# Kernel tuning notes

Measured on AMD Instinct MI355X. Metric: run time of the kernel, lower is better.

The kernel has to match this reference:

```python
import jax, jax.numpy as jnp
import numpy as np

B, S, Hd = 4, 2048, 1024
NH, D = 16, 64

def setup_inputs() -> dict:
    key = jax.random.key(0)
    ks = jax.random.split(key, 8)
    scale = 0.02
    return {
        "hidden_states": jax.random.normal(ks[0], (B, S, Hd), dtype=jnp.float32),
        "attention_mask": jnp.zeros((B, 1, 1, S), dtype=jnp.float32),
        "relations": jax.random.normal(ks[1], (1, 1, S, D), dtype=jnp.float32),
        "Wq": jax.random.normal(ks[2], (Hd, Hd), dtype=jnp.float32) * scale,
        "bq": jnp.zeros((Hd,), dtype=jnp.float32),
        "Wk": jax.random.normal(ks[3], (Hd, Hd), dtype=jnp.float32) * scale,
        "bk": jnp.zeros((Hd,), dtype=jnp.float32),
        "Wv": jax.random.normal(ks[4], (Hd, Hd), dtype=jnp.float32) * scale,
        "bv": jnp.zeros((Hd,), dtype=jnp.float32),
    }

def _heads(x):  # [B,S,Hd] -> [B,NH,S,D]
    return x.reshape(x.shape[0], x.shape[1], NH, D).transpose(0, 2, 1, 3)

def _rotate_half_interleaved(x):
    # stack([-x_odd, x_even], -1).reshape_as(x)
    return jnp.stack([-x[..., 1::2], x[..., ::2]], axis=-1).reshape(x.shape)

def reference(hidden_states, attention_mask, relations, Wq, bq, Wk, bk, Wv, bv):
    q = _heads(hidden_states @ Wq.T + bq)
    k = _heads(hidden_states @ Wk.T + bk)
    v = _heads(hidden_states @ Wv.T + bv)

    # interleaved rotary: cos from odd slots, sin from even slots, each repeated x2
    cos_pos = jnp.repeat(relations[..., 1::2], 2, axis=-1)  # [1,1,S,D]
    sin_pos = jnp.repeat(relations[..., ::2], 2, axis=-1)
    q = q * cos_pos + _rotate_half_interleaved(q) * sin_pos
    k = k * cos_pos + _rotate_half_interleaved(k) * sin_pos

    scores = jnp.einsum("bhqd,bhkd->bhqk", q, k) / jnp.sqrt(jnp.float32(D))
    scores = scores + attention_mask
    probs = jax.nn.softmax(scores, axis=-1)
    ctx = jnp.einsum("bhqk,bhkd->bhqd", probs, v)
    return ctx.transpose(0, 2, 1, 3).reshape(hidden_states.shape[0], hidden_states.shape[1], NH * D)
```

## Files before the change

kernel.cpp:

```cpp
#include <hip/hip_runtime.h>

typedef __attribute__((ext_vector_type(8))) short short8;
typedef __attribute__((ext_vector_type(4))) float f32x4;
typedef __attribute__((ext_vector_type(4))) unsigned int u32x4;
typedef __attribute__((ext_vector_type(2))) unsigned int u32x2;
typedef __attribute__((ext_vector_type(4))) unsigned short u16x4;

#define NHEADS 16
#define DHEAD 64
#define SEQ 2048
#define BATCH 4
#define HD 1024
#define MTOT 8192

static __device__ __forceinline__ unsigned short f2b(float x) {
  unsigned u = __builtin_bit_cast(unsigned, x);
  u += 0x7fffu + ((u >> 16) & 1u);
  return (unsigned short)(u >> 16);
}

static __device__ __forceinline__ unsigned pk2h(float lo, float hi) {
  unsigned a = __builtin_bit_cast(unsigned, lo) + 0x8000u;
  unsigned b = __builtin_bit_cast(unsigned, hi) + 0x8000u;
  return (a >> 16) | (b & 0xffff0000u);
}

static __device__ __forceinline__ void gll16(const void* g, void* l) {
  __builtin_amdgcn_global_load_lds(
      (const __attribute__((address_space(1))) unsigned int*)g,
      (__attribute__((address_space(3))) unsigned int*)l, 16, 0, 0);
}

__global__ void cvt_bf16(const float* __restrict__ src,
                         unsigned short* __restrict__ dst, int n4) {
  int i = blockIdx.x * blockDim.x + threadIdx.x;
  if (i < n4) {
    f32x4 v = ((const f32x4*)src)[i];
    u16x4 o;
    o[0] = f2b(v[0]); o[1] = f2b(v[1]); o[2] = f2b(v[2]); o[3] = f2b(v[3]);
    ((u16x4*)dst)[i] = o;
  }
}

#define WQ4 (HD * HD / 4)
__global__ void prep(const float* __restrict__ Wq, const float* __restrict__ Wk,
                     const float* __restrict__ Wv, const float* __restrict__ mask,
                     unsigned short* __restrict__ Wb,
                     unsigned short* __restrict__ Wm) {
  int i = blockIdx.x * blockDim.x + threadIdx.x;
  if (i < 3 * WQ4) {
    int rg = i / WQ4;
    int idx = i - rg * WQ4;
    const float* src = (rg == 0) ? Wq : (rg == 1) ? Wk : Wv;
    f32x4 v = ((const f32x4*)src)[idx];
    u16x4 o;
    o[0] = f2b(v[0]); o[1] = f2b(v[1]); o[2] = f2b(v[2]); o[3] = f2b(v[3]);
    ((u16x4*)(Wb + (size_t)rg * HD * HD))[idx] = o;
  } else {
    int j = i - 3 * WQ4;
    f32x4 v = ((const f32x4*)mask)[j];
    u16x4 o;
    o[0] = f2b(__expf(v[0])); o[1] = f2b(__expf(v[1]));
    o[2] = f2b(__expf(v[2])); o[3] = f2b(__expf(v[3]));
    ((u16x4*)Wm)[j] = o;
  }
}

__global__ __launch_bounds__(256) void qkv_gemm(
    const unsigned short* __restrict__ X,
    const unsigned short* __restrict__ Wall,
    const float* __restrict__ bq, const float* __restrict__ bk,
    const float* __restrict__ bv,
    const float* __restrict__ rel,
    const float* __restrict__ mask,
    unsigned short* __restrict__ Qo,
    unsigned short* __restrict__ Ko,
    unsigned short* __restrict__ Vt) {
  __shared__ __align__(16) unsigned short As[2][128 * 64];
  __shared__ __align__(16) unsigned short Bs[2][128 * 64];

  const int t = threadIdx.x;
  const int lane = t & 63;
  const int w = t >> 6;

  const int n = blockIdx.x;
  const int xcd = n & 7;
  const int li = n >> 3;
  const int bx = xcd * 8 + (li & 7);
  const int pp = li >> 3;
  const int by = pp & 7;
  const int bz = pp >> 3;

  const unsigned short* Wp = Wall + (size_t)bz * HD * HD;
  const int m0 = bx * 128;
  const int n0 = by * 128;

  const int cl = lane & 15;
  const int qd = lane >> 4;

  f32x4 acc[8][2];
#pragma unroll
  for (int i = 0; i < 8; i++)
#pragma unroll
    for (int j = 0; j < 2; j++) acc[i][j] = (f32x4){0.f, 0.f, 0.f, 0.f};

  auto stageA = [&](int b, int q, int k0) {
    int rr = (q << 5) + (t >> 3);
    gll16(X + (size_t)(m0 + rr) * HD + k0 + (((t & 7) ^ (rr & 7)) << 3),
          &As[b][((q << 5) + (w << 3)) * 64]);
  };
  auto stageB = [&](int b, int q, int k0) {
    int rr = (q << 5) + (t >> 3);
    gll16(Wp + (size_t)(n0 + rr) * HD + k0 + (((t & 7) ^ (rr & 7)) << 3),
          &Bs[b][((q << 5) + (w << 3)) * 64]);
  };

#define SYNC(N)                               \
  __builtin_amdgcn_sched_barrier(0);          \
  asm volatile("s_waitcnt vmcnt(" #N ")");    \
  __builtin_amdgcn_sched_barrier(0);          \
  __builtin_amdgcn_s_barrier();               \
  __builtin_amdgcn_sched_barrier(0);

  stageA(0, 0, 0); stageA(0, 1, 0);
  stageB(0, 0, 0); stageB(0, 1, 0);
  stageB(0, 2, 0); stageB(0, 3, 0);
  stageA(0, 2, 0); stageA(0, 3, 0);

#pragma unroll 1
  for (int it = 0; it < 16; it++) {
    const int bi = it & 1;
    const int nb = bi ^ 1;
    const int kn = ((it + 1) * 64) & 1023;
    const unsigned short* Asb = &As[bi][0];
    const unsigned short* Bsb = &Bs[bi][0];

    SYNC(2);

    stageA(nb, 0, kn); stageA(nb, 1, kn);
    stageB(nb, 0, kn); stageB(nb, 1, kn);

    short8 bf[2][2];
#pragma unroll
    for (int j = 0; j < 2; j++) {
      int r = w * 32 + j * 16 + cl;
      const unsigned short* rp = &Bsb[r * 64];
#pragma unroll
      for (int ks = 0; ks < 2; ks++)
        bf[j][ks] = *(const short8*)(rp + (((ks * 4 + qd) ^ (r & 7)) << 3));
    }

    __builtin_amdgcn_s_setprio(1);
#pragma unroll
    for (int mq = 0; mq < 2; mq++) {
#pragma unroll
      for (int ks = 0; ks < 2; ks++) {
        short8 af[2];
#pragma unroll
        for (int i = 0; i < 2; i++) {
          int r = mq * 32 + i * 16 + cl;
          af[i] = *(const short8*)(&Asb[r * 64] +
                                   (((ks * 4 + qd) ^ (r & 7)) << 3));
        }
        if (bz < 2) {
#pragma unroll
          for (int i = 0; i < 2; i++)
#pragma unroll
            for (int j = 0; j < 2; j++)
              acc[mq * 2 + i][j] = __builtin_amdgcn_mfma_f32_16x16x32_bf16(
                  bf[j][ks], af[i], acc[mq * 2 + i][j], 0, 0, 0);
        } else {
#pragma unroll
          for (int i = 0; i < 2; i++)
#pragma unroll
            for (int j = 0; j < 2; j++)
              acc[mq * 2 + i][j] = __builtin_amdgcn_mfma_f32_16x16x32_bf16(
                  af[i], bf[j][ks], acc[mq * 2 + i][j], 0, 0, 0);
        }
      }
    }
    __builtin_amdgcn_s_setprio(0);

    SYNC(4);

    stageB(nb, 2, kn); stageB(nb, 3, kn);
    stageA(nb, 2, kn); stageA(nb, 3, kn);

    __builtin_amdgcn_s_setprio(1);
#pragma unroll
    for (int mq = 2; mq < 4; mq++) {
#pragma unroll
      for (int ks = 0; ks < 2; ks++) {
        short8 af[2];
#pragma unroll
        for (int i = 0; i < 2; i++) {
          int r = mq * 32 + i * 16 + cl;
          af[i] = *(const short8*)(&Asb[r * 64] +
                                   (((ks * 4 + qd) ^ (r & 7)) << 3));
        }
        if (bz < 2) {
#pragma unroll
          for (int i = 0; i < 2; i++)
#pragma unroll
            for (int j = 0; j < 2; j++)
              acc[mq * 2 + i][j] = __builtin_amdgcn_mfma_f32_16x16x32_bf16(
                  bf[j][ks], af[i], acc[mq * 2 + i][j], 0, 0, 0);
        } else {
#pragma unroll
          for (int i = 0; i < 2; i++)
#pragma unroll
            for (int j = 0; j < 2; j++)
              acc[mq * 2 + i][j] = __builtin_amdgcn_mfma_f32_16x16x32_bf16(
                  af[i], bf[j][ks], acc[mq * 2 + i][j], 0, 0, 0);
        }
      }
    }
    __builtin_amdgcn_s_setprio(0);
  }
#undef SYNC

  if (bz == 2) {
#pragma unroll
    for (int mf = 0; mf < 8; mf++) {
      int mb = m0 + mf * 16 + qd * 4;
      int bb = mb >> 11, ssb = mb & (SEQ - 1);
      f32x4 mk = *(const f32x4*)(mask + bb * SEQ + ssb);
      f32x4 w4;
#pragma unroll
      for (int r = 0; r < 4; r++) w4[r] = __expf(mk[r]);
      int colp = (ssb & ~31) | ((ssb & 12) << 1) | (((ssb >> 4) & 1) << 2);
#pragma unroll
      for (int nf = 0; nf < 2; nf++) {
        int feat = n0 + w * 32 + nf * 16 + cl;
        int hh = feat >> 6;
        int dd = feat & 63;
        float bn = bv[feat];
        u32x2 pk;
        pk[0] = pk2h((acc[mf][nf][0] + bn) * w4[0], (acc[mf][nf][1] + bn) * w4[1]);
        pk[1] = pk2h((acc[mf][nf][2] + bn) * w4[2], (acc[mf][nf][3] + bn) * w4[3]);
        *(u32x2*)(Vt + ((size_t)((bb * NHEADS + hh) * DHEAD + dd)) * SEQ + colp) = pk;
      }
    }
  } else {
    const float* bias = (bz == 0) ? bq : bk;
    unsigned short* Out = (bz == 0) ? Qo : Ko;
    const float qs = (bz == 0) ? 0.125f * 1.4426950408889634f : 1.0f;
#pragma unroll
    for (int nf = 0; nf < 2; nf++) {
      int feat0 = n0 + w * 32 + nf * 16 + qd * 4;
      int hh = feat0 >> 6;
      int ddb = feat0 & 63;
      f32x4 b4 = *(const f32x4*)(bias + feat0);
#pragma unroll
      for (int mf = 0; mf < 8; mf++) {
        int s = m0 + mf * 16 + cl;
        int bb = s >> 11, ss = s & (SEQ - 1);
        f32x4 rl = *(const f32x4*)(rel + ss * DHEAD + ddb);
        float x0 = acc[mf][nf][0] + b4[0];
        float x1 = acc[mf][nf][1] + b4[1];
        float x2 = acc[mf][nf][2] + b4[2];
        float x3 = acc[mf][nf][3] + b4[3];
        float y0 = (x0 * rl[1] - x1 * rl[0]) * qs;
        float y1 = (x1 * rl[1] + x0 * rl[0]) * qs;
        float y2 = (x2 * rl[3] - x3 * rl[2]) * qs;
        float y3 = (x3 * rl[3] + x2 * rl[2]) * qs;
        u32x2 pk;
        pk[0] = pk2h(y0, y1);
        pk[1] = pk2h(y2, y3);
        *(u32x2*)(Out + (((size_t)(bb * NHEADS + hh)) * SEQ + ss) * DHEAD + ddb) = pk;
      }
    }
  }
}

__global__ __launch_bounds__(256, 2) void attn(
    const unsigned short* __restrict__ Q,
    const unsigned short* __restrict__ K,
    const unsigned short* __restrict__ Vt,
    const unsigned short* __restrict__ wmask,
    float* __restrict__ out) {
  __shared__ __align__(16) unsigned short Ks[128 * 64];
  __shared__ __align__(16) unsigned short Vs[64 * 128];

  const int t = threadIdx.x;
  const int lane = t & 63;
  const int w = t >> 6;

  const int n = blockIdx.x;
  const int xcd = n & 7;
  const int li = n >> 3;
  const int bh = xcd * 8 + (li >> 4);
  const int qt = li & 15;

  const int b = bh >> 4, h = bh & 15;
  const int s0 = qt * 128;
  const unsigned short* Qp = Q + (size_t)bh * SEQ * DHEAD;
  const unsigned short* Kp = K + (size_t)bh * SEQ * DHEAD;
  const unsigned short* Vp = Vt + (size_t)bh * DHEAD * SEQ;
  const unsigned short* wmp = wmask + b * SEQ;

  const int cl = lane & 15;
  const int qd = lane >> 4;

  short8 qf[2][2];
#pragma unroll
  for (int mt = 0; mt < 2; mt++)
#pragma unroll
    for (int ks = 0; ks < 2; ks++)
      qf[mt][ks] = *(const short8*)(Qp + (size_t)(s0 + w * 32 + mt * 16 + cl) * DHEAD +
                                    ks * 32 + qd * 8);

  f32x4 ov[2][4];
  f32x4 ovl[2];
#pragma unroll
  for (int mt = 0; mt < 2; mt++) {
    ovl[mt] = (f32x4){0.f, 0.f, 0.f, 0.f};
#pragma unroll
    for (int dt = 0; dt < 4; dt++) ov[mt][dt] = (f32x4){0.f, 0.f, 0.f, 0.f};
  }

  auto stageK = [&](int kt) {
#pragma unroll
    for (int j = 0; j < 4; j++) {
      int r0 = w * 32 + j * 8;
      int r = r0 + (lane >> 3);
      int c = (lane & 7) ^ (r & 7);
      gll16(Kp + (size_t)(kt + r) * DHEAD + c * 8, &Ks[r0 * 64]);
    }
  };
  auto stageV = [&](int kt) {
#pragma unroll
    for (int j = 0; j < 4; j++) {
      int r0 = w * 16 + j * 4;
      int r = r0 + (lane >> 4);
      int c = (lane & 15) ^ (r & 7);
      gll16(Vp + (size_t)r * SEQ + kt + c * 8, &Vs[r0 * 128]);
    }
  };

  stageK(0);

  for (int it = 0; it < SEQ / 128; it++) {
    const int kt = it * 128;
    __syncthreads();
    stageV(kt);

    short8 wf[4];
#pragma unroll
    for (int c = 0; c < 4; c++) {
      u32x2 w0 = *(const u32x2*)(wmp + kt + c * 32 + qd * 4);
      u32x2 w1 = *(const u32x2*)(wmp + kt + c * 32 + 16 + qd * 4);
      u32x4 ww = {w0[0], w0[1], w1[0], w1[1]};
      wf[c] = __builtin_bit_cast(short8, ww);
    }

    f32x4 sc[2][8];
#pragma unroll
    for (int mt = 0; mt < 2; mt++)
#pragma unroll
      for (int nt = 0; nt < 8; nt++) sc[mt][nt] = (f32x4){0.f, 0.f, 0.f, 0.f};
#pragma unroll
    for (int ks = 0; ks < 2; ks++) {
#pragma unroll
      for (int nt = 0; nt < 8; nt++) {
        int krow = nt * 16 + cl;
        short8 kf = *(const short8*)(Ks + krow * 64 +
                                     (((ks * 4 + qd) ^ (krow & 7)) << 3));
        sc[0][nt] = __builtin_amdgcn_mfma_f32_16x16x32_bf16(kf, qf[0][ks], sc[0][nt], 0, 0, 0);
        sc[1][nt] = __builtin_amdgcn_mfma_f32_16x16x32_bf16(kf, qf[1][ks], sc[1][nt], 0, 0, 0);
      }
    }

    unsigned pw[2][8][2];
#pragma unroll
    for (int mt = 0; mt < 2; mt++) {
#pragma unroll
      for (int nt = 0; nt < 8; nt++) {
        float p0 = __builtin_amdgcn_exp2f(sc[mt][nt][0]);
        float p1 = __builtin_amdgcn_exp2f(sc[mt][nt][1]);
        float p2 = __builtin_amdgcn_exp2f(sc[mt][nt][2]);
        float p3 = __builtin_amdgcn_exp2f(sc[mt][nt][3]);
        pw[mt][nt][0] = pk2h(p0, p1);
        pw[mt][nt][1] = pk2h(p2, p3);
      }
    }

    __builtin_amdgcn_sched_barrier(0);
    asm volatile("s_waitcnt vmcnt(0)");
    __builtin_amdgcn_sched_barrier(0);
    __builtin_amdgcn_s_barrier();
    __builtin_amdgcn_sched_barrier(0);

    if (it + 1 < SEQ / 128) stageK(kt + 128);

#pragma unroll
    for (int c = 0; c < 4; c++) {
      u32x4 bb0 = {pw[0][2 * c][0], pw[0][2 * c][1], pw[0][2 * c + 1][0], pw[0][2 * c + 1][1]};
      u32x4 bb1 = {pw[1][2 * c][0], pw[1][2 * c][1], pw[1][2 * c + 1][0], pw[1][2 * c + 1][1]};
      short8 bf0 = __builtin_bit_cast(short8, bb0);
      short8 bf1 = __builtin_bit_cast(short8, bb1);
      ovl[0] = __builtin_amdgcn_mfma_f32_16x16x32_bf16(wf[c], bf0, ovl[0], 0, 0, 0);
      ovl[1] = __builtin_amdgcn_mfma_f32_16x16x32_bf16(wf[c], bf1, ovl[1], 0, 0, 0);
#pragma unroll
      for (int dt = 0; dt < 4; dt++) {
        int vrow = dt * 16 + cl;
        short8 vf = *(const short8*)(Vs + vrow * 128 +
                                     (((c * 4 + qd) ^ (vrow & 7)) << 3));
        ov[0][dt] = __builtin_amdgcn_mfma_f32_16x16x32_bf16(vf, bf0, ov[0][dt], 0, 0, 0);
        ov[1][dt] = __builtin_amdgcn_mfma_f32_16x16x32_bf16(vf, bf1, ov[1][dt], 0, 0, 0);
      }
    }
  }

#pragma unroll
  for (int mt = 0; mt < 2; mt++) {
    float rl = 1.0f / ovl[mt][0];
    int s = s0 + w * 32 + mt * 16 + cl;
    float* ob = out + ((size_t)b * SEQ + s) * HD + h * DHEAD;
#pragma unroll
    for (int dt = 0; dt < 4; dt++) {
      f32x4 o;
      o[0] = ov[mt][dt][0] * rl;
      o[1] = ov[mt][dt][1] * rl;
      o[2] = ov[mt][dt][2] * rl;
      o[3] = ov[mt][dt][3] * rl;
      *(f32x4*)(ob + dt * 16 + qd * 4) = o;
    }
  }
}

extern "C" void kernel_launch(void* const* d_in, const int* in_sizes, int n_in,
                              void* d_out, int out_size, void* d_ws, size_t ws_size,
                              hipStream_t stream) {
  const float* hidden = (const float*)d_in[0];
  const float* mask   = (const float*)d_in[1];
  const float* rel    = (const float*)d_in[2];
  const float* Wq     = (const float*)d_in[3];
  const float* bq     = (const float*)d_in[4];
  const float* Wk     = (const float*)d_in[5];
  const float* bk     = (const float*)d_in[6];
  const float* Wv     = (const float*)d_in[7];
  const float* bv     = (const float*)d_in[8];
  float* out = (float*)d_out;

  unsigned short* Xb = (unsigned short*)d_ws;
  unsigned short* Wb = Xb + (size_t)MTOT * HD;
  unsigned short* Qb = Wb + (size_t)3 * HD * HD;
  unsigned short* Kb = Qb + (size_t)MTOT * HD;
  unsigned short* Vb = Kb + (size_t)MTOT * HD;
  unsigned short* Wm = Vb + (size_t)MTOT * HD;

  {
    int n4 = MTOT * HD / 4;
    cvt_bf16<<<n4 / 256, 256, 0, stream>>>(hidden, Xb, n4);
  }
  prep<<<(3 * WQ4 + BATCH * SEQ / 4) / 256, 256, 0, stream>>>(Wq, Wk, Wv, mask, Wb, Wm);
  qkv_gemm<<<dim3(1536), 256, 0, stream>>>(Xb, Wb, bq, bk, bv, rel, mask, Qb, Kb, Vb);
  attn<<<dim3(1024), 256, 0, stream>>>(Qb, Kb, Vb, Wm, out);
}
```

Measured before the change: 267.5 us.

## Replace double-buffered QKV GEMM pipeline with single-buffered load-then-compute loop

Drops the two-stage LDS double buffer and the split half-tile prefetch schedule in the QKV projection GEMM. Each k-step now loads the full A and B tiles, synchronizes, then runs all MFMAs. This halves LDS usage, which may allow more resident blocks. In exchange, global loads no longer overlap with matrix math, and correct waiting on the async LDS loads relies on the barrier semantics.

```diff
diff --git a/kernel.cpp b/kernel.cpp
--- a/kernel.cpp
+++ b/kernel.cpp
@@ -76,8 +76,8 @@
     unsigned short* __restrict__ Qo,
     unsigned short* __restrict__ Ko,
     unsigned short* __restrict__ Vt) {
-  __shared__ __align__(16) unsigned short As[2][128 * 64];
-  __shared__ __align__(16) unsigned short Bs[2][128 * 64];
+  __shared__ __align__(16) unsigned short As[128 * 64];
+  __shared__ __align__(16) unsigned short Bs[128 * 64];
 
   const int t = threadIdx.x;
   const int lane = t & 63;
@@ -104,47 +104,30 @@
 #pragma unroll
     for (int j = 0; j < 2; j++) acc[i][j] = (f32x4){0.f, 0.f, 0.f, 0.f};
 
-  auto stageA = [&](int b, int q, int k0) {
+  auto stageA = [&](int q, int k0) {
     int rr = (q << 5) + (t >> 3);
     gll16(X + (size_t)(m0 + rr) * HD + k0 + (((t & 7) ^ (rr & 7)) << 3),
-          &As[b][((q << 5) + (w << 3)) * 64]);
+          &As[((q << 5) + (w << 3)) * 64]);
   };
-  auto stageB = [&](int b, int q, int k0) {
+  auto stageB = [&](int q, int k0) {
     int rr = (q << 5) + (t >> 3);
     gll16(Wp + (size_t)(n0 + rr) * HD + k0 + (((t & 7) ^ (rr & 7)) << 3),
-          &Bs[b][((q << 5) + (w << 3)) * 64]);
+          &Bs[((q << 5) + (w << 3)) * 64]);
   };
-
-#define SYNC(N)                               \
-  __builtin_amdgcn_sched_barrier(0);          \
-  asm volatile("s_waitcnt vmcnt(" #N ")");    \
-  __builtin_amdgcn_sched_barrier(0);          \
-  __builtin_amdgcn_s_barrier();               \
-  __builtin_amdgcn_sched_barrier(0);
-
-  stageA(0, 0, 0); stageA(0, 1, 0);
-  stageB(0, 0, 0); stageB(0, 1, 0);
-  stageB(0, 2, 0); stageB(0, 3, 0);
-  stageA(0, 2, 0); stageA(0, 3, 0);
 
 #pragma unroll 1
   for (int it = 0; it < 16; it++) {
-    const int bi = it & 1;
-    const int nb = bi ^ 1;
-    const int kn = ((it + 1) * 64) & 1023;
-    const unsigned short* Asb = &As[bi][0];
-    const unsigned short* Bsb = &Bs[bi][0];
-
-    SYNC(2);
-
-    stageA(nb, 0, kn); stageA(nb, 1, kn);
-    stageB(nb, 0, kn); stageB(nb, 1, kn);
+    const int k0 = it * 64;
+    __syncthreads();
+    stageA(0, k0); stageA(1, k0); stageA(2, k0); stageA(3, k0);
+    stageB(0, k0); stageB(1, k0); stageB(2, k0); stageB(3, k0);
+    __syncthreads();
 
     short8 bf[2][2];
 #pragma unroll
     for (int j = 0; j < 2; j++) {
       int r = w * 32 + j * 16 + cl;
-      const unsigned short* rp = &Bsb[r * 64];
+      const unsigned short* rp = &Bs[r * 64];
 #pragma unroll
       for (int ks = 0; ks < 2; ks++)
         bf[j][ks] = *(const short8*)(rp + (((ks * 4 + qd) ^ (r & 7)) << 3));
@@ -152,14 +135,14 @@
 
     __builtin_amdgcn_s_setprio(1);
 #pragma unroll
-    for (int mq = 0; mq < 2; mq++) {
+    for (int mq = 0; mq < 4; mq++) {
 #pragma unroll
       for (int ks = 0; ks < 2; ks++) {
         short8 af[2];
 #pragma unroll
         for (int i = 0; i < 2; i++) {
           int r = mq * 32 + i * 16 + cl;
-          af[i] = *(const short8*)(&Asb[r * 64] +
+          af[i] = *(const short8*)(&As[r * 64] +
                                    (((ks * 4 + qd) ^ (r & 7)) << 3));
         }
         if (bz < 2) {
@@ -180,44 +163,7 @@
       }
     }
     __builtin_amdgcn_s_setprio(0);
-
-    SYNC(4);
-
-    stageB(nb, 2, kn); stageB(nb, 3, kn);
-    stageA(nb, 2, kn); stageA(nb, 3, kn);
-
-    __builtin_amdgcn_s_setprio(1);
-#pragma unroll
-    for (int mq = 2; mq < 4; mq++) {
-#pragma unroll
-      for (int ks = 0; ks < 2; ks++) {
-        short8 af[2];
-#pragma unroll
-        for (int i = 0; i < 2; i++) {
-          int r = mq * 32 + i * 16 + cl;
-          af[i] = *(const short8*)(&Asb[r * 64] +
-                                   (((ks * 4 + qd) ^ (r & 7)) << 3));
-        }
-        if (bz < 2) {
-#pragma unroll
-          for (int i = 0; i < 2; i++)
-#pragma unroll
-            for (int j = 0; j < 2; j++)
-              acc[mq * 2 + i][j] = __builtin_amdgcn_mfma_f32_16x16x32_bf16(
-                  bf[j][ks], af[i], acc[mq * 2 + i][j], 0, 0, 0);
-        } else {
-#pragma unroll
-          for (int i = 0; i < 2; i++)
-#pragma unroll
-            for (int j = 0; j < 2; j++)
-              acc[mq * 2 + i][j] = __builtin_amdgcn_mfma_f32_16x16x32_bf16(
-                  af[i], bf[j][ks], acc[mq * 2 + i][j], 0, 0, 0);
-        }
-      }
-    }
-    __builtin_amdgcn_s_setprio(0);
-  }
-#undef SYNC
+  }
 
   if (bz == 2) {
 #pragma unroll
```

After: 252.9 us. 1.06x faster.
